# Kernel optimization log

Hardware: AMD Instinct MI355X
Metric: run time of the kernel (lower is better)

Reference implementation:

```python
import jax, jax.numpy as jnp
import numpy as np

B, S, D, H = 4, 2048, 256, 8
HD = D // H
SCALE = float(np.sqrt(HD))  # temperature = head_dim ** 0.5


def setup_inputs() -> dict:
    key = jax.random.key(0)
    ks = jax.random.split(key, 12)
    w = lambda k, shape: jax.random.normal(k, shape, dtype=jnp.float32) * 0.05
    x = jax.random.normal(ks[0], (B, S, D), dtype=jnp.float32)
    adj = jax.random.randint(ks[1], (B, S, S), 0, 2, dtype=jnp.int32)
    return {
        "x": x,
        "adj": adj,
        "w_qkv": w(ks[2], (3 * D, D)),
        "b_qkv": jnp.zeros((3 * D,), jnp.float32),
        "ln_g": jnp.ones((D,), jnp.float32),
        "ln_b": jnp.zeros((D,), jnp.float32),
        "w_fc": w(ks[3], (D, D)),
        "b_fc": jnp.zeros((D,), jnp.float32),
        "w_z": w(ks[4], (D, D)),
        "b_z": jnp.full((D,), -2.0, jnp.float32),  # init_bias fills w_z bias with -2
        "u_z": w(ks[5], (D, D)),
        "w_r": w(ks[6], (D, D)),
        "u_r": w(ks[7], (D, D)),
        "w_g": w(ks[8], (D, D)),
        "u_g": w(ks[9], (D, D)),
    }


def reference(x, adj, w_qkv, b_qkv, ln_g, ln_b, w_fc, b_fc,
              w_z, b_z, u_z, w_r, u_r, w_g, u_g):
    residual = x
    # LayerNorm (eps=1e-5, torch default)
    mu = jnp.mean(x, axis=-1, keepdims=True)
    var = jnp.var(x, axis=-1, keepdims=True)
    xn = (x - mu) / jnp.sqrt(var + 1e-5) * ln_g + ln_b
    # fused QKV projection -> (B*H, S, 3*HD), batch-major over (b, h)
    qkv = xn @ w_qkv.T + b_qkv                       # [B,S,3D]
    qkv = qkv.reshape(B, S, H, 3 * HD).transpose(0, 2, 1, 3).reshape(B * H, S, 3 * HD)
    q, k, v = jnp.split(qkv, 3, axis=-1)
    # masked scaled dot-product attention (full NxN scores, as in original)
    attn = jnp.einsum('nqd,nkd->nqk', q, k) / SCALE  # [B*H,S,S]
    adj_r = jnp.repeat(adj, H, axis=0)               # batch-major, matches attn layout
    attn = jnp.where(adj_r == 0, -jnp.inf, attn)
    attn = jax.nn.softmax(attn, axis=-1)
    out = jnp.einsum('nqk,nkd->nqd', attn, v)        # [B*H,S,HD]
    # Faithful replication of torch's view(n_head, batch, ...) applied to
    # batch-major data (an ordering quirk in the original module).
    out = out.reshape(H, B, S, HD).transpose(1, 2, 0, 3).reshape(B, S, D)
    y = jax.nn.relu(out @ w_fc.T + b_fc)
    # GRU gate: x=residual, y=attention branch
    z = jax.nn.sigmoid(y @ w_z.T + b_z + residual @ u_z.T)
    r = jax.nn.sigmoid(y @ w_r.T + residual @ u_r.T)
    h_hat = jnp.tanh(y @ w_g.T + (r * residual) @ u_g.T)
    return (1.0 - z) * residual + z * h_hat
```

## Files before the change

### kernel.cpp

```cpp
#include <hip/hip_runtime.h>
#include <hip/hip_bf16.h>
#include <math.h>

#define B_  4
#define S_  2048
#define D_  256
#define H_  8
#define HD_ 32
#define QSCALE 0.25504175929589786f

typedef short  bf16x8 __attribute__((ext_vector_type(8)));
typedef float  f32x4  __attribute__((ext_vector_type(4)));
typedef unsigned short ushort_t;
typedef unsigned int   uint_t;

__device__ __forceinline__ ushort_t f2b(float f) {
    union { float f; unsigned u; } v; v.f = f;
    unsigned r = (v.u + 0x7FFFu + ((v.u >> 16) & 1u)) >> 16;
    return (ushort_t)r;
}
__device__ __forceinline__ float b2f(ushort_t s) {
    return __uint_as_float((uint_t)s << 16);
}

__device__ __forceinline__ float wave_sum(float v) {
#pragma unroll
    for (int o = 32; o > 0; o >>= 1) v += __shfl_down(v, o, 64);
    return v;
}
__device__ __forceinline__ float block_sum256(float v, float* scr) {
    v = wave_sum(v);
    int lane = threadIdx.x & 63, wid = threadIdx.x >> 6;
    if (lane == 0) scr[wid] = v;
    __syncthreads();
    float r = scr[0] + scr[1] + scr[2] + scr[3];
    __syncthreads();
    return r;
}

#define WQ_SZ 196608
#define WS_SZ 65536
#define NB_ADJ 8192
#define NB_WC  2560
#define NB_LN  8192
__global__ __launch_bounds__(256)
void prep_kernel(const int* __restrict__ adj, uint_t* __restrict__ bits,
                 const float* __restrict__ w0, const float* __restrict__ w1,
                 const float* __restrict__ w2, const float* __restrict__ w3,
                 const float* __restrict__ w4, const float* __restrict__ w5,
                 const float* __restrict__ w6, const float* __restrict__ w7,
                 ushort_t* __restrict__ wout,
                 const float* __restrict__ x, const float* __restrict__ g,
                 const float* __restrict__ bb, ushort_t* __restrict__ xn_b) {
    __shared__ float scr[4];
    int blk = blockIdx.x, tid = threadIdx.x;
    if (blk < NB_ADJ) {
        int lane = tid & 63;
#pragma unroll
        for (int gp = 0; gp < 8; ++gp) {
            size_t i = ((size_t)blk * 8 + gp) * 256 + tid;
            unsigned long long m = __ballot(adj[i] != 0);
            size_t wbase = (((size_t)blk * 8 + gp) * 256 + (tid & ~63)) >> 5;
            if (lane == 0)  bits[wbase]     = (uint_t)m;
            if (lane == 32) bits[wbase + 1] = (uint_t)(m >> 32);
        }
    } else if (blk < NB_ADJ + NB_WC) {
        int idx = (blk - NB_ADJ) * 256 + tid;
        const float* src; int o;
        if (idx < WQ_SZ) { src = w0; o = idx; }
        else {
            int j = idx - WQ_SZ, seg = j >> 16; o = j & (WS_SZ - 1);
            src = (seg == 0) ? w1 : (seg == 1) ? w2 : (seg == 2) ? w3 :
                  (seg == 3) ? w4 : (seg == 4) ? w5 : (seg == 5) ? w6 : w7;
        }
        int j  = o & 7;
        int l  = (o >> 3) & 15;
        int qd = (o >> 7) & 3;
        int ks = (o >> 9) & 7;
        int ct = o >> 12;
        wout[idx] = f2b(src[(ct * 16 + l) * 256 + ks * 32 + qd * 8 + j]);
    } else {
        size_t base = (size_t)(blk - NB_ADJ - NB_WC) * D_;
        float v  = x[base + tid];
        float mu = block_sum256(v, scr) * (1.0f / D_);
        float d  = v - mu;
        float var = block_sum256(d * d, scr) * (1.0f / D_);
        float rstd = rsqrtf(var + 1e-5f);
        xn_b[base + tid] = f2b(d * rstd * g[tid] + bb[tid]);
    }
}

__global__ __launch_bounds__(256)
void gemm_qkv(const ushort_t* __restrict__ A, const ushort_t* __restrict__ Wf,
              const float* __restrict__ bias, ushort_t* __restrict__ outb,
              ushort_t* __restrict__ vT) {
    __shared__ ushort_t Sa[64][264];
    int tid = threadIdx.x;
    int wave = tid >> 6, lane = tid & 63, l = lane & 15, quad = lane >> 4;
    int wm = wave >> 1, wn = wave & 1;
    int m0 = blockIdx.y * 64, n0 = blockIdx.x * 64;
    {
        int row = tid >> 2, c0 = (tid & 3) * 64;
        const ushort_t* ap = A + (size_t)(m0 + row) * 256 + c0;
#pragma unroll
        for (int j = 0; j < 8; ++j)
            *(uint4*)&Sa[row][c0 + 8 * j] = ((const uint4*)ap)[j];
    }
    __syncthreads();

    bf16x8 af[2][8];
#pragma unroll
    for (int mt = 0; mt < 2; ++mt)
#pragma unroll
        for (int ks = 0; ks < 8; ++ks)
            af[mt][ks] = *(const bf16x8*)&Sa[wm * 32 + mt * 16 + l][ks * 32 + quad * 8];

    f32x4 acc[2][2];
#pragma unroll
    for (int i = 0; i < 2; ++i)
#pragma unroll
        for (int j = 0; j < 2; ++j) acc[i][j] = (f32x4){0.f, 0.f, 0.f, 0.f};

#pragma unroll
    for (int nt = 0; nt < 2; ++nt) {
        int ct = (n0 >> 4) + wn * 2 + nt;
        bf16x8 wfr[8];
#pragma unroll
        for (int ks = 0; ks < 8; ++ks)
            wfr[ks] = *(const bf16x8*)(Wf + (((size_t)ct * 8 + ks) * 64 + lane) * 8);
#pragma unroll
        for (int ks = 0; ks < 8; ++ks) {
            acc[0][nt] = __builtin_amdgcn_mfma_f32_16x16x32_bf16(af[0][ks], wfr[ks], acc[0][nt], 0, 0, 0);
            acc[1][nt] = __builtin_amdgcn_mfma_f32_16x16x32_bf16(af[1][ks], wfr[ks], acc[1][nt], 0, 0, 0);
        }
    }

    __syncthreads();
    ushort_t* So = &Sa[0][0];
#pragma unroll
    for (int nt = 0; nt < 2; ++nt) {
        int col = wn * 32 + nt * 16 + l;
        int gcol = n0 + col;
        float bv = bias[gcol];
        float qs = ((gcol % 96) < 32) ? QSCALE : 1.0f;
#pragma unroll
        for (int mt = 0; mt < 2; ++mt)
#pragma unroll
            for (int r = 0; r < 4; ++r) {
                int row = wm * 32 + mt * 16 + quad * 4 + r;
                So[row * 72 + col] = f2b((acc[mt][nt][r] + bv) * qs);
            }
    }
    __syncthreads();
    {
        int row = tid >> 2, seg = tid & 3;
        uint4 v0 = *(uint4*)&So[row * 72 + seg * 16];
        uint4 v1 = *(uint4*)&So[row * 72 + seg * 16 + 8];
        ushort_t* op = outb + (size_t)(m0 + row) * 768 + n0 + seg * 16;
        ((uint4*)op)[0] = v0;
        ((uint4*)op)[1] = v1;
    }

    int vs = n0 % 96;
    if (vs != 0) {
        int vloc = (vs == 64) ? 0 : 32;
        int h  = (n0 + vloc) / 96;
        int b  = m0 >> 11;
        int s0 = m0 & (S_ - 1);
        ushort_t* vstage = &Sa[0][0] + 8192;
        {
            int c = tid & 31, seg = tid >> 5;
            ushort_t tmp[8];
#pragma unroll
            for (int i = 0; i < 8; ++i)
                tmp[i] = So[(seg * 8 + i) * 72 + vloc + c];
            uint_t u[4];
#pragma unroll
            for (int i = 0; i < 4; ++i)
                u[i] = (uint_t)tmp[2 * i] | ((uint_t)tmp[2 * i + 1] << 16);
            *(uint4*)&vstage[c * 72 + seg * 8] = make_uint4(u[0], u[1], u[2], u[3]);
        }
        __syncthreads();
        {
            int d = tid >> 3, tseg = tid & 7;
            uint4 v = *(uint4*)&vstage[d * 72 + tseg * 8];
            *(uint4*)&vT[((size_t)(b * 8 + h) * 32 + d) * S_ + s0 + tseg * 8] = v;
        }
    }
}

__global__ __launch_bounds__(256)
void fused_gate(const ushort_t* __restrict__ attn_b, const float* __restrict__ xf,
                const ushort_t* __restrict__ wfc, const ushort_t* __restrict__ wz,
                const ushort_t* __restrict__ uz, const ushort_t* __restrict__ wr,
                const ushort_t* __restrict__ ur, const ushort_t* __restrict__ wg,
                const ushort_t* __restrict__ ug, const float* __restrict__ bfc,
                const float* __restrict__ bz, float* __restrict__ out) {
    __shared__ ushort_t Sa[16][264];
    __shared__ ushort_t Sx[16][264];
    __shared__ ushort_t Sy[16][264];
    __shared__ ushort_t St[16][264];
    int tid = threadIdx.x;
    int wave = tid >> 6, lane = tid & 63, l = lane & 15, quad = lane >> 4;
    int m0 = blockIdx.x * 16;
    int colbase = wave * 64;

    {
        int row = tid >> 4, c0 = (tid & 15) * 16;
        const ushort_t* ap = attn_b + (size_t)(m0 + row) * 256 + c0;
        uint4 a0 = ((const uint4*)ap)[0];
        uint4 a1 = ((const uint4*)ap)[1];
        *(uint4*)&Sa[row][c0] = a0;
        *(uint4*)&Sa[row][c0 + 8] = a1;
        const float4* xp = (const float4*)(xf + (size_t)(m0 + row) * 256 + c0);
        float4 f0 = xp[0], f1 = xp[1], f2_ = xp[2], f3 = xp[3];
        union { __hip_bfloat162 h[4]; uint4 u; } p0, p1;
        p0.h[0] = __float22bfloat162_rn(make_float2(f0.x, f0.y));
        p0.h[1] = __float22bfloat162_rn(make_float2(f0.z, f0.w));
        p0.h[2] = __float22bfloat162_rn(make_float2(f1.x, f1.y));
        p0.h[3] = __float22bfloat162_rn(make_float2(f1.z, f1.w));
        p1.h[0] = __float22bfloat162_rn(make_float2(f2_.x, f2_.y));
        p1.h[1] = __float22bfloat162_rn(make_float2(f2_.z, f2_.w));
        p1.h[2] = __float22bfloat162_rn(make_float2(f3.x, f3.y));
        p1.h[3] = __float22bfloat162_rn(make_float2(f3.z, f3.w));
        *(uint4*)&Sx[row][c0]     = p0.u;
        *(uint4*)&Sx[row][c0 + 8] = p1.u;
    }
    __syncthreads();

    {
        bf16x8 af[8];
#pragma unroll
        for (int ks = 0; ks < 8; ++ks)
            af[ks] = *(const bf16x8*)&Sa[l][ks * 32 + quad * 8];
        f32x4 ya[4];
#pragma unroll
        for (int nt = 0; nt < 4; ++nt) ya[nt] = (f32x4){0.f, 0.f, 0.f, 0.f};
#pragma unroll
        for (int nt = 0; nt < 4; ++nt) {
            size_t fb = ((size_t)(wave * 4 + nt) * 8) * 512 + lane * 8;
#pragma unroll
            for (int ks = 0; ks < 8; ++ks) {
                bf16x8 wfr = *(const bf16x8*)(wfc + fb + ks * 512);
                ya[nt] = __builtin_amdgcn_mfma_f32_16x16x32_bf16(af[ks], wfr, ya[nt], 0, 0, 0);
            }
        }
#pragma unroll
        for (int nt = 0; nt < 4; ++nt) {
            int col = colbase + nt * 16 + l;
            float bv = bfc[col];
#pragma unroll
            for (int r = 0; r < 4; ++r)
                Sy[quad * 4 + r][col] = f2b(fmaxf(ya[nt][r] + bv, 0.0f));
        }
    }
    __syncthreads();

    f32x4 az[4], ar[4], ag[4];
#pragma unroll
    for (int nt = 0; nt < 4; ++nt) {
        az[nt] = (f32x4){0.f, 0.f, 0.f, 0.f};
        ar[nt] = (f32x4){0.f, 0.f, 0.f, 0.f};
        ag[nt] = (f32x4){0.f, 0.f, 0.f, 0.f};
    }
#pragma unroll
    for (int nt = 0; nt < 4; ++nt) {
        size_t fb = ((size_t)(wave * 4 + nt) * 8) * 512 + lane * 8;
#pragma unroll
        for (int ks = 0; ks < 8; ++ks) {
            bf16x8 fy = *(const bf16x8*)&Sy[l][ks * 32 + quad * 8];
            bf16x8 fx = *(const bf16x8*)&Sx[l][ks * 32 + quad * 8];
            bf16x8 fz  = *(const bf16x8*)(wz + fb + ks * 512);
            bf16x8 fuz = *(const bf16x8*)(uz + fb + ks * 512);
            bf16x8 fr  = *(const bf16x8*)(wr + fb + ks * 512);
            bf16x8 fur = *(const bf16x8*)(ur + fb + ks * 512);
            bf16x8 fg  = *(const bf16x8*)(wg + fb + ks * 512);
            az[nt] = __builtin_amdgcn_mfma_f32_16x16x32_bf16(fy, fz,  az[nt], 0, 0, 0);
            az[nt] = __builtin_amdgcn_mfma_f32_16x16x32_bf16(fx, fuz, az[nt], 0, 0, 0);
            ar[nt] = __builtin_amdgcn_mfma_f32_16x16x32_bf16(fy, fr,  ar[nt], 0, 0, 0);
            ar[nt] = __builtin_amdgcn_mfma_f32_16x16x32_bf16(fx, fur, ar[nt], 0, 0, 0);
            ag[nt] = __builtin_amdgcn_mfma_f32_16x16x32_bf16(fy, fg,  ag[nt], 0, 0, 0);
        }
    }
#pragma unroll
    for (int nt = 0; nt < 4; ++nt) {
        int col = colbase + nt * 16 + l;
        float bzv = bz[col];
#pragma unroll
        for (int r = 0; r < 4; ++r) {
            int row = quad * 4 + r;
            az[nt][r] = 1.0f / (1.0f + __expf(-(az[nt][r] + bzv)));
            float rr  = 1.0f / (1.0f + __expf(-ar[nt][r]));
            St[row][col] = f2b(rr * b2f(Sx[row][col]));
        }
    }
    __syncthreads();

    f32x4 fcc[4];
#pragma unroll
    for (int nt = 0; nt < 4; ++nt) fcc[nt] = (f32x4){0.f, 0.f, 0.f, 0.f};
#pragma unroll
    for (int nt = 0; nt < 4; ++nt) {
        size_t fb = ((size_t)(wave * 4 + nt) * 8) * 512 + lane * 8;
#pragma unroll
        for (int ks = 0; ks < 8; ++ks) {
            bf16x8 ft = *(const bf16x8*)&St[l][ks * 32 + quad * 8];
            bf16x8 fu = *(const bf16x8*)(ug + fb + ks * 512);
            fcc[nt] = __builtin_amdgcn_mfma_f32_16x16x32_bf16(ft, fu, fcc[nt], 0, 0, 0);
        }
    }
#pragma unroll
    for (int nt = 0; nt < 4; ++nt) {
        int col = colbase + nt * 16 + l;
#pragma unroll
        for (int r = 0; r < 4; ++r) {
            int row = quad * 4 + r;
            float v = ag[nt][r] + fcc[nt][r];
            float e = __expf(2.0f * v);
            float h = 1.0f - 2.0f / (e + 1.0f);
            float zz = az[nt][r];
            size_t idx = (size_t)(m0 + row) * 256 + col;
            out[idx] = (1.0f - zz) * xf[idx] + zz * h;
        }
    }
}

__global__ __launch_bounds__(256)
void attn_kernel(const ushort_t* __restrict__ qkvb, const ushort_t* __restrict__ vT,
                 const uint_t* __restrict__ abits, ushort_t* __restrict__ attn_b) {
    __shared__ ushort_t Ks[64][40];
    __shared__ ushort_t Vt[32][72];
    __shared__ ushort_t Ps[64][72];
    __shared__ uint2   lut[16];

    int tid = threadIdx.x;
    int wave = tid >> 6, lane = tid & 63, l = lane & 15, quad = lane >> 4;
    int q0 = blockIdx.x * 64;
    int n  = blockIdx.y;
    int b = n >> 3, h = n & 7;
    int bp = n & 3, hp = n >> 2;

    if (tid < 16)
        lut[tid] = make_uint2(((tid & 1) ? 0xFFFFu : 0u) | ((tid & 2) ? 0xFFFF0000u : 0u),
                              ((tid & 4) ? 0xFFFFu : 0u) | ((tid & 8) ? 0xFFFF0000u : 0u));

    const ushort_t* base = qkvb + (size_t)b * S_ * 768 + h * 96;
    int myq = wave * 16 + l;
    int qsh = quad * 4;

    bf16x8 qf = *(const bf16x8*)(base + (size_t)(q0 + myq) * 768 + quad * 8);

    bf16x8 ones;
#pragma unroll
    for (int i = 0; i < 8; ++i) ones[i] = (short)0x3F80;

    f32x4 oacc[2], aones;
    oacc[0] = (f32x4){0.f, 0.f, 0.f, 0.f};
    oacc[1] = (f32x4){0.f, 0.f, 0.f, 0.f};
    aones   = (f32x4){0.f, 0.f, 0.f, 0.f};

    int skey = tid >> 2, spart = tid & 3;
    int kcol = (spart * 8) ^ (((skey >> 3) & 1) << 3);
    int vd = tid >> 3, vk = (tid & 7) * 8;
    const ushort_t* vptr = vT + ((size_t)n * 32 + vd) * S_ + vk;
    const uint_t* aptr = abits + ((size_t)b * S_ + q0 + myq) * 64;

    uint4 kv = *(const uint4*)(base + (size_t)skey * 768 + 32 + spart * 8);
    uint4 vv = *(const uint4*)(vptr);
    uint2 aw = *(const uint2*)(aptr);

    for (int k0 = 0; k0 < S_; k0 += 64) {
        __syncthreads();
        *(uint4*)&Ks[skey][kcol] = kv;
        *(uint4*)&Vt[vd][vk] = vv;
        uint_t aw0 = aw.x, aw1 = aw.y;
        if (k0 + 64 < S_) {
            kv = *(const uint4*)(base + (size_t)(k0 + 64 + skey) * 768 + 32 + spart * 8);
            vv = *(const uint4*)(vptr + k0 + 64);
            aw = *(const uint2*)(aptr + ((k0 + 64) >> 5));
        }
        __syncthreads();

#pragma unroll
        for (int t4 = 0; t4 < 4; ++t4) {
            bf16x8 kf = *(const bf16x8*)&Ks[t4 * 16 + l][(quad * 8) ^ ((l >> 3) << 3)];
            f32x4 z = (f32x4){0.f, 0.f, 0.f, 0.f};
            f32x4 sc = __builtin_amdgcn_mfma_f32_16x16x32_bf16(kf, qf, z, 0, 0, 0);
            uint_t w = (t4 & 2) ? aw1 : aw0;
            uint_t idx = (w >> ((t4 & 1) * 16 + qsh)) & 15u;
            uint2 mk = lut[idx];
            union { __hip_bfloat162 b2[2]; uint2 u2; } pk;
            pk.b2[0] = __float22bfloat162_rn(make_float2(exp2f(sc[0]), exp2f(sc[1])));
            pk.b2[1] = __float22bfloat162_rn(make_float2(exp2f(sc[2]), exp2f(sc[3])));
            pk.u2.x &= mk.x;
            pk.u2.y &= mk.y;
            *(uint2*)&Ps[myq][t4 * 16 + qsh] = pk.u2;
        }

#pragma unroll
        for (int ks = 0; ks < 2; ++ks) {
            bf16x8 pf = *(const bf16x8*)&Ps[wave * 16 + l][ks * 32 + quad * 8];
            aones = __builtin_amdgcn_mfma_f32_16x16x32_bf16(ones, pf, aones, 0, 0, 0);
#pragma unroll
            for (int mt = 0; mt < 2; ++mt) {
                bf16x8 vf = *(const bf16x8*)&Vt[mt * 16 + l][ks * 32 + quad * 8];
                oacc[mt] = __builtin_amdgcn_mfma_f32_16x16x32_bf16(vf, pf, oacc[mt], 0, 0, 0);
            }
        }
    }

    float linv = 1.0f / aones[0];

    __syncthreads();
    ushort_t* Ost = &Ks[0][0];
#pragma unroll
    for (int mt = 0; mt < 2; ++mt)
#pragma unroll
        for (int r = 0; r < 4; ++r)
            Ost[myq * 40 + mt * 16 + quad * 4 + r] = f2b(oacc[mt][r] * linv);
    __syncthreads();
    {
        int q = tid >> 2, part = tid & 3;
        uint4 v = *(uint4*)&Ost[q * 40 + part * 8];
        *(uint4*)&attn_b[((size_t)(bp * S_ + q0 + q)) * 256 + hp * 32 + part * 8] = v;
    }
}

extern "C" void kernel_launch(void* const* d_in, const int* in_sizes, int n_in,
                              void* d_out, int out_size, void* d_ws, size_t ws_size,
                              hipStream_t stream) {
    const float* x     = (const float*)d_in[0];
    const int*   adj   = (const int*)d_in[1];
    const float* w_qkv = (const float*)d_in[2];
    const float* b_qkv = (const float*)d_in[3];
    const float* ln_g  = (const float*)d_in[4];
    const float* ln_b  = (const float*)d_in[5];
    const float* w_fc  = (const float*)d_in[6];
    const float* b_fc  = (const float*)d_in[7];
    const float* w_z   = (const float*)d_in[8];
    const float* b_z   = (const float*)d_in[9];
    const float* u_z   = (const float*)d_in[10];
    const float* w_r   = (const float*)d_in[11];
    const float* u_r   = (const float*)d_in[12];
    const float* w_g   = (const float*)d_in[13];
    const float* u_g   = (const float*)d_in[14];
    float* out = (float*)d_out;

    const size_t TOK  = (size_t)B_ * S_;
    const size_t TOKD = TOK * D_;
    ushort_t* xn_b   = (ushort_t*)d_ws;
    ushort_t* qkv_b  = xn_b + TOKD;
    ushort_t* attn_b = qkv_b + TOK * 768;
    ushort_t* wb     = attn_b + TOKD;
    uint_t*   bits   = (uint_t*)(wb + WQ_SZ + 7 * WS_SZ);
    ushort_t* vTb    = (ushort_t*)(bits + (size_t)B_ * S_ * S_ / 32);

    ushort_t* wq_b  = wb;
    ushort_t* wfc_b = wb + WQ_SZ;
    ushort_t* wz_b  = wfc_b + WS_SZ;
    ushort_t* uz_b  = wz_b + WS_SZ;
    ushort_t* wr_b  = uz_b + WS_SZ;
    ushort_t* ur_b  = wr_b + WS_SZ;
    ushort_t* wg_b  = ur_b + WS_SZ;
    ushort_t* ug_b  = wg_b + WS_SZ;

    prep_kernel<<<NB_ADJ + NB_WC + NB_LN, 256, 0, stream>>>(
        adj, bits, w_qkv, w_fc, w_z, u_z, w_r, u_r, w_g, u_g, wb,
        x, ln_g, ln_b, xn_b);

    gemm_qkv<<<dim3(12, 128), 256, 0, stream>>>(xn_b, wq_b, b_qkv, qkv_b, vTb);

    attn_kernel<<<dim3(S_ / 64, B_ * H_), 256, 0, stream>>>(qkv_b, vTb, bits, attn_b);

    fused_gate<<<512, 256, 0, stream>>>(
        attn_b, x, wfc_b, wz_b, uz_b, wr_b, ur_b, wg_b, ug_b, b_fc, b_z, out);
}
```

Before: 239.9 us.

## Split attention over key halves and combine partial sums in gate kernel

Splits the attention kernel's key loop into two halves as separate blocks, doubling the grid from 1024 to 2048 blocks. Each half writes unnormalized fp32 partial outputs and row sums to workspace. The fused gate kernel sums the two partials, normalizes, and converts to bf16 on load. The aim is more parallelism and better occupancy on the GPU, at the cost of extra fp32 global traffic for the partial buffers. The shared-memory padding of Vt and Ps is also changed from 72 to 74.

```diff
diff --git a/kernel.cpp b/kernel.cpp
--- a/kernel.cpp
+++ b/kernel.cpp
@@ -8,6 +8,7 @@
 #define H_  8
 #define HD_ 32
 #define QSCALE 0.25504175929589786f
+#define TOKD_ 2097152
 
 typedef short  bf16x8 __attribute__((ext_vector_type(8)));
 typedef float  f32x4  __attribute__((ext_vector_type(4)));
@@ -190,7 +191,8 @@
 }
 
 __global__ __launch_bounds__(256)
-void fused_gate(const ushort_t* __restrict__ attn_b, const float* __restrict__ xf,
+void fused_gate(const float* __restrict__ partO, const float* __restrict__ partL,
+                const float* __restrict__ xf,
                 const ushort_t* __restrict__ wfc, const ushort_t* __restrict__ wz,
                 const ushort_t* __restrict__ uz, const ushort_t* __restrict__ wr,
                 const ushort_t* __restrict__ ur, const ushort_t* __restrict__ wg,
@@ -207,12 +209,31 @@
 
     {
         int row = tid >> 4, c0 = (tid & 15) * 16;
-        const ushort_t* ap = attn_b + (size_t)(m0 + row) * 256 + c0;
-        uint4 a0 = ((const uint4*)ap)[0];
-        uint4 a1 = ((const uint4*)ap)[1];
-        *(uint4*)&Sa[row][c0] = a0;
-        *(uint4*)&Sa[row][c0 + 8] = a1;
-        const float4* xp = (const float4*)(xf + (size_t)(m0 + row) * 256 + c0);
+        int t = m0 + row;
+        int bp = t >> 11, q = t & (S_ - 1);
+        int n = (c0 >> 5) * 4 + bp;
+        float2 lp = *(const float2*)&partL[((size_t)n * S_ + q) * 2];
+        float linv = 1.0f / (lp.x + lp.y);
+        const float4* o0 = (const float4*)(partO + (size_t)t * 256 + c0);
+        const float4* o1 = (const float4*)(partO + TOKD_ + (size_t)t * 256 + c0);
+        union { __hip_bfloat162 h[4]; uint4 u; } a0, a1;
+#pragma unroll
+        for (int i = 0; i < 2; ++i) {
+            float4 s0 = o0[2 * i],     s1 = o1[2 * i];
+            float4 s2 = o0[2 * i + 1], s3 = o1[2 * i + 1];
+            float2 p0 = make_float2((s0.x + s1.x) * linv, (s0.y + s1.y) * linv);
+            float2 p1 = make_float2((s0.z + s1.z) * linv, (s0.w + s1.w) * linv);
+            float2 p2 = make_float2((s2.x + s3.x) * linv, (s2.y + s3.y) * linv);
+            float2 p3 = make_float2((s2.z + s3.z) * linv, (s2.w + s3.w) * linv);
+            (i ? a1 : a0).h[0] = __float22bfloat162_rn(p0);
+            (i ? a1 : a0).h[1] = __float22bfloat162_rn(p1);
+            (i ? a1 : a0).h[2] = __float22bfloat162_rn(p2);
+            (i ? a1 : a0).h[3] = __float22bfloat162_rn(p3);
+        }
+        *(uint4*)&Sa[row][c0]     = a0.u;
+        *(uint4*)&Sa[row][c0 + 8] = a1.u;
+
+        const float4* xp = (const float4*)(xf + (size_t)t * 256 + c0);
         float4 f0 = xp[0], f1 = xp[1], f2_ = xp[2], f3 = xp[3];
         union { __hip_bfloat162 h[4]; uint4 u; } p0, p1;
         p0.h[0] = __float22bfloat162_rn(make_float2(f0.x, f0.y));
@@ -327,18 +348,21 @@
 
 __global__ __launch_bounds__(256)
 void attn_kernel(const ushort_t* __restrict__ qkvb, const ushort_t* __restrict__ vT,
-                 const uint_t* __restrict__ abits, ushort_t* __restrict__ attn_b) {
+                 const uint_t* __restrict__ abits, float* __restrict__ partO,
+                 float* __restrict__ partL) {
     __shared__ ushort_t Ks[64][40];
-    __shared__ ushort_t Vt[32][72];
-    __shared__ ushort_t Ps[64][72];
+    __shared__ ushort_t Vt[32][74];
+    __shared__ ushort_t Ps[64][74];
     __shared__ uint2   lut[16];
 
     int tid = threadIdx.x;
     int wave = tid >> 6, lane = tid & 63, l = lane & 15, quad = lane >> 4;
     int q0 = blockIdx.x * 64;
-    int n  = blockIdx.y;
+    int n2 = blockIdx.y;
+    int n = n2 >> 1, kh = n2 & 1;
     int b = n >> 3, h = n & 7;
     int bp = n & 3, hp = n >> 2;
+    int k0beg = kh << 10, k0end = k0beg + 1024;
 
     if (tid < 16)
         lut[tid] = make_uint2(((tid & 1) ? 0xFFFFu : 0u) | ((tid & 2) ? 0xFFFF0000u : 0u),
@@ -365,16 +389,16 @@
     const ushort_t* vptr = vT + ((size_t)n * 32 + vd) * S_ + vk;
     const uint_t* aptr = abits + ((size_t)b * S_ + q0 + myq) * 64;
 
-    uint4 kv = *(const uint4*)(base + (size_t)skey * 768 + 32 + spart * 8);
-    uint4 vv = *(const uint4*)(vptr);
-    uint2 aw = *(const uint2*)(aptr);
-
-    for (int k0 = 0; k0 < S_; k0 += 64) {
+    uint4 kv = *(const uint4*)(base + (size_t)(k0beg + skey) * 768 + 32 + spart * 8);
+    uint4 vv = *(const uint4*)(vptr + k0beg);
+    uint2 aw = *(const uint2*)(aptr + (k0beg >> 5));
+
+    for (int k0 = k0beg; k0 < k0end; k0 += 64) {
         __syncthreads();
         *(uint4*)&Ks[skey][kcol] = kv;
         *(uint4*)&Vt[vd][vk] = vv;
         uint_t aw0 = aw.x, aw1 = aw.y;
-        if (k0 + 64 < S_) {
+        if (k0 + 64 < k0end) {
             kv = *(const uint4*)(base + (size_t)(k0 + 64 + skey) * 768 + 32 + spart * 8);
             vv = *(const uint4*)(vptr + k0 + 64);
             aw = *(const uint2*)(aptr + ((k0 + 64) >> 5));
@@ -409,20 +433,25 @@
         }
     }
 
-    float linv = 1.0f / aones[0];
-
-    __syncthreads();
-    ushort_t* Ost = &Ks[0][0];
+    if (lane < 16)
+        partL[((size_t)n * S_ + q0 + myq) * 2 + kh] = aones[0];
+
+    __syncthreads();
+    float* Of = (float*)&Ps[0][0];
 #pragma unroll
     for (int mt = 0; mt < 2; ++mt)
 #pragma unroll
         for (int r = 0; r < 4; ++r)
-            Ost[myq * 40 + mt * 16 + quad * 4 + r] = f2b(oacc[mt][r] * linv);
+            Of[myq * 37 + mt * 16 + quad * 4 + r] = oacc[mt][r];
     __syncthreads();
     {
         int q = tid >> 2, part = tid & 3;
-        uint4 v = *(uint4*)&Ost[q * 40 + part * 8];
-        *(uint4*)&attn_b[((size_t)(bp * S_ + q0 + q)) * 256 + hp * 32 + part * 8] = v;
+        float4 v0 = *(float4*)&Of[q * 37 + part * 8];
+        float4 v1 = *(float4*)&Of[q * 37 + part * 8 + 4];
+        float* op = partO + (size_t)kh * TOKD_ +
+                    ((size_t)(bp * S_ + q0 + q)) * 256 + hp * 32 + part * 8;
+        ((float4*)op)[0] = v0;
+        ((float4*)op)[1] = v1;
     }
 }
 
@@ -450,10 +479,11 @@
     const size_t TOKD = TOK * D_;
     ushort_t* xn_b   = (ushort_t*)d_ws;
     ushort_t* qkv_b  = xn_b + TOKD;
-    ushort_t* attn_b = qkv_b + TOK * 768;
-    ushort_t* wb     = attn_b + TOKD;
+    ushort_t* wb     = qkv_b + TOK * 768;
     uint_t*   bits   = (uint_t*)(wb + WQ_SZ + 7 * WS_SZ);
     ushort_t* vTb    = (ushort_t*)(bits + (size_t)B_ * S_ * S_ / 32);
+    float*    partO  = (float*)(vTb + (size_t)1024 * S_);
+    float*    partL  = partO + 2 * TOKD;
 
     ushort_t* wq_b  = wb;
     ushort_t* wfc_b = wb + WQ_SZ;
@@ -470,8 +500,9 @@
 
     gemm_qkv<<<dim3(12, 128), 256, 0, stream>>>(xn_b, wq_b, b_qkv, qkv_b, vTb);
 
-    attn_kernel<<<dim3(S_ / 64, B_ * H_), 256, 0, stream>>>(qkv_b, vTb, bits, attn_b);
+    attn_kernel<<<dim3(S_ / 64, B_ * H_ * 2), 256, 0, stream>>>(
+        qkv_b, vTb, bits, partO, partL);
 
     fused_gate<<<512, 256, 0, stream>>>(
-        attn_b, x, wfc_b, wz_b, uz_b, wr_b, ur_b, wg_b, ug_b, b_fc, b_z, out);
-}
+        partO, partL, x, wfc_b, wz_b, uz_b, wr_b, ur_b, wg_b, ug_b, b_fc, b_z, out);
+}
```

New measurement: 252.3 us. +5.2%, slower.

## Load K/V fragments directly from global memory and drop LDS staging barriers

Applied to the files above, without the earlier changes.

The attention kernel no longer stages K and V tiles through shared memory with two block-wide barriers per key tile. Each wave now loads its own K and V MFMA fragments straight from global memory, and only the wave-private P tile stays in LDS, padded to a new row stride. This removes the per-iteration synchronisation and the LDS round trip. In exchange, each of the four waves fetches the same K/V data, which quadruples requests to L1/L2. The explicit register prefetch of the next tile is also gone, so load latency may be exposed.

```diff
diff --git a/kernel.cpp b/kernel.cpp
--- a/kernel.cpp
+++ b/kernel.cpp
@@ -328,9 +328,7 @@
 __global__ __launch_bounds__(256)
 void attn_kernel(const ushort_t* __restrict__ qkvb, const ushort_t* __restrict__ vT,
                  const uint_t* __restrict__ abits, ushort_t* __restrict__ attn_b) {
-    __shared__ ushort_t Ks[64][40];
-    __shared__ ushort_t Vt[32][72];
-    __shared__ ushort_t Ps[64][72];
+    __shared__ ushort_t Ps[64][74];
     __shared__ uint2   lut[16];
 
     int tid = threadIdx.x;
@@ -343,6 +341,7 @@
     if (tid < 16)
         lut[tid] = make_uint2(((tid & 1) ? 0xFFFFu : 0u) | ((tid & 2) ? 0xFFFF0000u : 0u),
                               ((tid & 4) ? 0xFFFFu : 0u) | ((tid & 8) ? 0xFFFF0000u : 0u));
+    __syncthreads();
 
     const ushort_t* base = qkvb + (size_t)b * S_ * 768 + h * 96;
     int myq = wave * 16 + l;
@@ -359,34 +358,28 @@
     oacc[1] = (f32x4){0.f, 0.f, 0.f, 0.f};
     aones   = (f32x4){0.f, 0.f, 0.f, 0.f};
 
-    int skey = tid >> 2, spart = tid & 3;
-    int kcol = (spart * 8) ^ (((skey >> 3) & 1) << 3);
-    int vd = tid >> 3, vk = (tid & 7) * 8;
-    const ushort_t* vptr = vT + ((size_t)n * 32 + vd) * S_ + vk;
-    const uint_t* aptr = abits + ((size_t)b * S_ + q0 + myq) * 64;
-
-    uint4 kv = *(const uint4*)(base + (size_t)skey * 768 + 32 + spart * 8);
-    uint4 vv = *(const uint4*)(vptr);
-    uint2 aw = *(const uint2*)(aptr);
+    const ushort_t* krow = base + (size_t)l * 768 + 32 + quad * 8;
+    const ushort_t* vrow = vT + ((size_t)n * 32 + l) * S_ + quad * 8;
+    const uint_t*   aptr = abits + ((size_t)b * S_ + q0 + myq) * 64;
 
     for (int k0 = 0; k0 < S_; k0 += 64) {
-        __syncthreads();
-        *(uint4*)&Ks[skey][kcol] = kv;
-        *(uint4*)&Vt[vd][vk] = vv;
-        uint_t aw0 = aw.x, aw1 = aw.y;
-        if (k0 + 64 < S_) {
-            kv = *(const uint4*)(base + (size_t)(k0 + 64 + skey) * 768 + 32 + spart * 8);
-            vv = *(const uint4*)(vptr + k0 + 64);
-            aw = *(const uint2*)(aptr + ((k0 + 64) >> 5));
-        }
-        __syncthreads();
+        bf16x8 kf[4];
+#pragma unroll
+        for (int t4 = 0; t4 < 4; ++t4)
+            kf[t4] = *(const bf16x8*)(krow + (size_t)(k0 + t4 * 16) * 768);
+        bf16x8 vf[2][2];
+#pragma unroll
+        for (int ks = 0; ks < 2; ++ks)
+#pragma unroll
+            for (int mt = 0; mt < 2; ++mt)
+                vf[ks][mt] = *(const bf16x8*)(vrow + (size_t)mt * 16 * S_ + k0 + ks * 32);
+        uint2 aw = *(const uint2*)(aptr + (k0 >> 5));
 
 #pragma unroll
         for (int t4 = 0; t4 < 4; ++t4) {
-            bf16x8 kf = *(const bf16x8*)&Ks[t4 * 16 + l][(quad * 8) ^ ((l >> 3) << 3)];
             f32x4 z = (f32x4){0.f, 0.f, 0.f, 0.f};
-            f32x4 sc = __builtin_amdgcn_mfma_f32_16x16x32_bf16(kf, qf, z, 0, 0, 0);
-            uint_t w = (t4 & 2) ? aw1 : aw0;
+            f32x4 sc = __builtin_amdgcn_mfma_f32_16x16x32_bf16(kf[t4], qf, z, 0, 0, 0);
+            uint_t w = (t4 & 2) ? aw.y : aw.x;
             uint_t idx = (w >> ((t4 & 1) * 16 + qsh)) & 15u;
             uint2 mk = lut[idx];
             union { __hip_bfloat162 b2[2]; uint2 u2; } pk;
@@ -402,17 +395,15 @@
             bf16x8 pf = *(const bf16x8*)&Ps[wave * 16 + l][ks * 32 + quad * 8];
             aones = __builtin_amdgcn_mfma_f32_16x16x32_bf16(ones, pf, aones, 0, 0, 0);
 #pragma unroll
-            for (int mt = 0; mt < 2; ++mt) {
-                bf16x8 vf = *(const bf16x8*)&Vt[mt * 16 + l][ks * 32 + quad * 8];
-                oacc[mt] = __builtin_amdgcn_mfma_f32_16x16x32_bf16(vf, pf, oacc[mt], 0, 0, 0);
-            }
+            for (int mt = 0; mt < 2; ++mt)
+                oacc[mt] = __builtin_amdgcn_mfma_f32_16x16x32_bf16(vf[ks][mt], pf, oacc[mt], 0, 0, 0);
         }
     }
 
     float linv = 1.0f / aones[0];
 
     __syncthreads();
-    ushort_t* Ost = &Ks[0][0];
+    ushort_t* Ost = &Ps[0][0];
 #pragma unroll
     for (int mt = 0; mt < 2; ++mt)
 #pragma unroll
```

Measured after the change: 307.2 us. +28.1%, slower.
